# Optimization experiments

Hardware: AMD Instinct MI355X
Metric: run time of the kernel (lower is better)

Reference implementation:

```python
import jax, jax.numpy as jnp
import numpy as np

B, NN, HIS, MSG = 16, 1000, 12, 64
NODE_DIM, EDGE_DIM, META_DIM = 32, 16, 128
GAT_DIM = HIS * MSG            # 768
META_IN = NODE_DIM + GAT_DIM   # 800
N = B * NN                     # 16000 total nodes
E = 128000
NEG_SLOPE = 0.2


def setup_inputs() -> dict:
    key = jax.random.key(0)
    ks = jax.random.split(key, 16)
    def glorot(k, shape):
        fan_in = shape[0]
        lim = 1.0 / np.sqrt(fan_in)
        return jax.random.uniform(k, shape, jnp.float32, -lim, lim)
    return {
        "node_feature": jax.random.normal(ks[0], (B, NN, NODE_DIM), jnp.float32),
        "edge_attr": jax.random.normal(ks[1], (E, EDGE_DIM), jnp.float32),
        "message_feature": jax.random.normal(ks[2], (B, NN, HIS, MSG), jnp.float32),
        "edge_index": jax.random.randint(ks[3], (2, E), 0, N, jnp.int64) if jax.config.jax_enable_x64 else jax.random.randint(ks[3], (2, E), 0, N, jnp.int32),
        # node_learner / edge_learner
        "W_node": glorot(ks[4], (NODE_DIM, NODE_DIM)),
        "b_node": jnp.zeros((NODE_DIM,), jnp.float32),
        "W_edge": glorot(ks[5], (EDGE_DIM, EDGE_DIM)),
        "b_edge": jnp.zeros((EDGE_DIM,), jnp.float32),
        # GATConv(768, 768, heads=1, concat=False)
        "W_gat": glorot(ks[6], (GAT_DIM, GAT_DIM)),
        "att_src": glorot(ks[7], (GAT_DIM,)) * 0.1,
        "att_dst": glorot(ks[8], (GAT_DIM,)) * 0.1,
        "b_gat": jnp.zeros((GAT_DIM,), jnp.float32),
        # GNNConv([meta_in, meta_dim], dim=edge_dim)
        "W_nbr": glorot(ks[9], (2 * META_IN + EDGE_DIM, META_DIM)),
        "b_nbr": jnp.zeros((META_DIM,), jnp.float32),
        "W_self": glorot(ks[10], (META_IN, META_DIM)),
        "b_self": jnp.zeros((META_DIM,), jnp.float32),
    }


def reference(node_feature, edge_attr, message_feature, edge_index,
              W_node, b_node, W_edge, b_edge,
              W_gat, att_src, att_dst, b_gat,
              W_nbr, b_nbr, W_self, b_self):
    src, dst = edge_index[0], edge_index[1]  # j -> i

    # node / edge learners
    nf = (node_feature @ W_node + b_node).reshape(-1, NODE_DIM)        # [N, 32]
    ea = edge_attr @ W_edge + b_edge                                   # [E, 16]
    mf = message_feature.reshape(-1, GAT_DIM)                          # [N, 768]

    # --- GATConv (1 head, concat=False, add_self_loops=True, eval: no dropout) ---
    loops = jnp.arange(N, dtype=src.dtype)
    src_sl = jnp.concatenate([src, loops])
    dst_sl = jnp.concatenate([dst, loops])
    h = mf @ W_gat                                                     # [N, 768]
    a_src = h @ att_src                                                # [N]
    a_dst = h @ att_dst                                                # [N]
    alpha = jax.nn.leaky_relu(a_src[src_sl] + a_dst[dst_sl], NEG_SLOPE)  # [E+N]
    amax = jax.ops.segment_max(alpha, dst_sl, num_segments=N)
    ex = jnp.exp(alpha - amax[dst_sl])
    denom = jax.ops.segment_sum(ex, dst_sl, num_segments=N)
    coef = ex / denom[dst_sl]
    gat_out = jax.ops.segment_sum(h[src_sl] * coef[:, None], dst_sl, num_segments=N) + b_gat

    # --- meta input + GNNConv (aggr='add', batch_norm=False) ---
    x = jnp.concatenate([gat_out, nf], axis=-1)                        # [N, 800]
    z = jnp.concatenate([x[dst], x[src], ea], axis=-1)                 # [E, 1616]
    msg = z @ W_nbr + b_nbr                                            # [E, 128]
    agg = jax.ops.segment_sum(msg, dst, num_segments=N)                # [N, 128]
    out = agg + x @ W_self + b_self                                    # [N, 128]
    return out.reshape(-1, NN, META_DIM)                               # [B, 1000, 128]
```

## Files before the change

kernel.cpp:

```cpp
#include <hip/hip_runtime.h>

#define N_NODES 16000
#define N_EDGES 128000
#define GATD 768
#define NODED 32
#define EDGED 16
#define METAIN 800
#define METAD 128
#define YCOLS 384

typedef short s16x8 __attribute__((ext_vector_type(8)));
typedef float f32x4v __attribute__((ext_vector_type(4)));

__device__ __forceinline__ unsigned short f2bf(float f){
    unsigned u = __float_as_uint(f);
    return (unsigned short)((u + 0x7fffu + ((u >> 16) & 1u)) >> 16);
}
__device__ __forceinline__ float us2f(unsigned short u){ return __uint_as_float(((unsigned)u)<<16); }

__device__ __forceinline__ void gload16(const void* g, void* l){
    __builtin_amdgcn_global_load_lds((const __attribute__((address_space(1))) void*)g,
                                     (__attribute__((address_space(3))) void*)l, 16, 0, 0);
}

__global__ __launch_bounds__(256) void pack_all_kernel(const float* __restrict__ W_gat,
                                                       const float* __restrict__ W_nbr,
                                                       const float* __restrict__ W_self,
                                                       const float* __restrict__ W_edge,
                                                       const float* __restrict__ b_edge,
                                                       unsigned short* __restrict__ WgT,
                                                       unsigned short* __restrict__ WcatT,
                                                       float* __restrict__ W16g,
                                                       float* __restrict__ bbg){
    int bid = blockIdx.x, tid = threadIdx.x;
    if (bid < 144){
        __shared__ float t[64][65];
        int bi = bid / 12, bj = bid % 12;
        int r16 = tid >> 4, c4 = (tid & 15) * 4;
        #pragma unroll
        for (int it = 0; it < 4; ++it){
            int row = it*16 + r16;
            float4 v = *reinterpret_cast<const float4*>(W_gat + (size_t)(bi*64+row)*GATD + bj*64 + c4);
            t[row][c4+0]=v.x; t[row][c4+1]=v.y; t[row][c4+2]=v.z; t[row][c4+3]=v.w;
        }
        __syncthreads();
        #pragma unroll
        for (int it = 0; it < 4; ++it){
            int row = it*16 + r16;
            ushort4 o;
            o.x = f2bf(t[c4+0][row]); o.y = f2bf(t[c4+1][row]);
            o.z = f2bf(t[c4+2][row]); o.w = f2bf(t[c4+3][row]);
            *reinterpret_cast<ushort4*>(WgT + (size_t)(bj*64+row)*GATD + bi*64 + c4) = o;
        }
    } else if (bid < 1344){
        int idx = (bid-144)*256 + tid;
        int c = idx / METAIN, k = idx % METAIN;
        float v;
        if (c < 128)      v = W_nbr[(size_t)k*METAD + c];
        else if (c < 256) v = W_nbr[(size_t)(800+k)*METAD + (c-128)];
        else              v = W_self[(size_t)k*METAD + (c-256)];
        WcatT[idx] = f2bf(v);
    } else {
        int c = tid;
        if (c < 128){
            float w3[16];
            #pragma unroll
            for (int k = 0; k < 16; ++k) w3[k] = W_nbr[(size_t)(1600+k)*METAD + c];
            #pragma unroll
            for (int j = 0; j < 16; ++j){
                float s = 0.f;
                #pragma unroll
                for (int k = 0; k < 16; ++k) s += W_edge[j*16+k] * w3[k];
                W16g[j*128 + c] = s;
            }
            float bb = 0.f;
            #pragma unroll
            for (int k = 0; k < 16; ++k) bb += b_edge[k] * w3[k];
            bbg[c] = bb;
        }
    }
}

__global__ __launch_bounds__(256) void nf_kernel(const float* __restrict__ node_feature,
                                                 const float* __restrict__ W_node,
                                                 const float* __restrict__ b_node,
                                                 unsigned short* __restrict__ x_bf){
    __shared__ float Wn[1024];
    __shared__ float bn[32];
    int tid = threadIdx.x;
    for (int i = tid; i < 1024; i += 256) Wn[i] = W_node[i];
    if (tid < 32) bn[tid] = b_node[tid];
    __syncthreads();
    int idx = blockIdx.x*256 + tid;
    int n = idx >> 5, j = idx & 31;
    const float* row = node_feature + (size_t)n*NODED;
    float s = bn[j];
    #pragma unroll
    for (int k = 0; k < 32; ++k) s += row[k] * Wn[k*32 + j];
    x_bf[(size_t)n*METAIN + GATD + j] = f2bf(s);
}


__global__ __launch_bounds__(256) void deg_kernel(const int* __restrict__ dst, int* __restrict__ deg){
    int e = blockIdx.x*256 + threadIdx.x;
    atomicAdd(&deg[dst[e]], 1);
}

__global__ __launch_bounds__(1024) void scan_kernel(const int* __restrict__ deg,
                                                    int* __restrict__ rowstart,
                                                    int* __restrict__ cursor){
    __shared__ int part[1024];
    int t = threadIdx.x;
    int base = t * 16;
    int local[16];
    int s = 0;
    #pragma unroll
    for (int k = 0; k < 16; ++k){
        int idx = base + k;
        int v = (idx < N_NODES) ? deg[idx] : 0;
        local[k] = s; s += v;
    }
    part[t] = s;
    __syncthreads();
    for (int off = 1; off < 1024; off <<= 1){
        int v = 0;
        if (t >= off) v = part[t-off];
        __syncthreads();
        if (t >= off) part[t] += v;
        __syncthreads();
    }
    int excl = (t == 0) ? 0 : part[t-1];
    #pragma unroll
    for (int k = 0; k < 16; ++k){
        int idx = base + k;
        if (idx < N_NODES){ int rs = excl + local[k]; rowstart[idx] = rs; cursor[idx] = rs; }
    }
    if (t == 1023) rowstart[N_NODES] = part[1023];
}

__global__ __launch_bounds__(256) void csr_kernel(const int* __restrict__ dst,
                                                  int* __restrict__ cursor,
                                                  int* __restrict__ csr){
    int e = blockIdx.x*256 + threadIdx.x;
    int p = atomicAdd(&cursor[dst[e]], 1);
    csr[p] = e;
}


template<bool AF32, bool DOTS, bool BFOUT>
__global__ __launch_bounds__(256) void mfma_gemm_kernel(const float* __restrict__ A32,
                                                        const unsigned short* __restrict__ A16,
                                                        const unsigned short* __restrict__ Bt,
                                                        float* __restrict__ Cf,
                                                        unsigned short* __restrict__ Cb,
                                                        const float* __restrict__ att_src,
                                                        const float* __restrict__ att_dst,
                                                        float* __restrict__ a_srcO,
                                                        float* __restrict__ a_dstO,
                                                        int Ncols, int K){
    __shared__ __align__(16) unsigned short As[128*32];
    __shared__ __align__(16) unsigned short Bs[128*32];
    int tid = threadIdx.x;
    int wave = tid >> 6, lane = tid & 63;
    int rowBase = blockIdx.y * 128, colBase = blockIdx.x * 128;
    const float*          gA32p = AF32 ? A32 + (size_t)(rowBase + (tid>>2))*K + (tid&3)*8 : nullptr;
    const unsigned short* gA16p = AF32 ? nullptr : A16 + (size_t)(rowBase + (tid>>2))*K + (tid&3)*8;
    const unsigned short* gBp   = Bt + (size_t)(colBase + (tid>>2))*K + (tid&3)*8;
    char* lA = (char*)As + tid*16;
    char* lB = (char*)Bs + tid*16;
    int r0 = (wave>>1)*64, c0 = (wave&1)*64;
    int rl = lane & 15, koff = (lane>>4)*8;
    f32x4v acc[4][4] = {};
    for (int k0 = 0; k0 < K; k0 += 32){
        __syncthreads();
        gload16(gBp + k0,                  lB);
        gload16(gBp + (size_t)64*K + k0,   lB + 4096);
        if constexpr (AF32){
            float4 a0 = *reinterpret_cast<const float4*>(gA32p + k0);
            float4 a1 = *reinterpret_cast<const float4*>(gA32p + k0 + 4);
            float4 a2 = *reinterpret_cast<const float4*>(gA32p + (size_t)64*K + k0);
            float4 a3 = *reinterpret_cast<const float4*>(gA32p + (size_t)64*K + k0 + 4);
            union { unsigned short u[8]; s16x8 v; } p0, p1;
            p0.u[0]=f2bf(a0.x); p0.u[1]=f2bf(a0.y); p0.u[2]=f2bf(a0.z); p0.u[3]=f2bf(a0.w);
            p0.u[4]=f2bf(a1.x); p0.u[5]=f2bf(a1.y); p0.u[6]=f2bf(a1.z); p0.u[7]=f2bf(a1.w);
            p1.u[0]=f2bf(a2.x); p1.u[1]=f2bf(a2.y); p1.u[2]=f2bf(a2.z); p1.u[3]=f2bf(a2.w);
            p1.u[4]=f2bf(a3.x); p1.u[5]=f2bf(a3.y); p1.u[6]=f2bf(a3.z); p1.u[7]=f2bf(a3.w);
            *reinterpret_cast<s16x8*>(lA)        = p0.v;
            *reinterpret_cast<s16x8*>(lA + 4096) = p1.v;
        } else {
            gload16(gA16p + k0,                lA);
            gload16(gA16p + (size_t)64*K + k0, lA + 4096);
        }
        __syncthreads();
        s16x8 af[4], bfr[4];
        #pragma unroll
        for (int mi = 0; mi < 4; ++mi)
            af[mi] = *reinterpret_cast<const s16x8*>(&As[(r0 + mi*16 + rl)*32 + koff]);
        #pragma unroll
        for (int ni = 0; ni < 4; ++ni)
            bfr[ni] = *reinterpret_cast<const s16x8*>(&Bs[(c0 + ni*16 + rl)*32 + koff]);
        #pragma unroll
        for (int mi = 0; mi < 4; ++mi)
            #pragma unroll
            for (int ni = 0; ni < 4; ++ni)
                acc[mi][ni] = __builtin_amdgcn_mfma_f32_16x16x32_bf16(af[mi], bfr[ni], acc[mi][ni], 0, 0, 0);
    }
    int orow = rowBase + r0 + (lane>>4)*4;
    int ocol = colBase + c0 + rl;
    #pragma unroll
    for (int mi = 0; mi < 4; ++mi)
        #pragma unroll
        for (int ni = 0; ni < 4; ++ni){
            #pragma unroll
            for (int j = 0; j < 4; ++j){
                size_t idx = (size_t)(orow + mi*16 + j)*Ncols + ocol + ni*16;
                if constexpr (BFOUT) Cb[idx] = f2bf(acc[mi][ni][j]);
                else                 Cf[idx] = acc[mi][ni][j];
            }
        }
    if constexpr (DOTS){
        float as_c[4], ad_c[4];
        #pragma unroll
        for (int ni = 0; ni < 4; ++ni){
            int col = colBase + c0 + ni*16 + rl;
            as_c[ni] = att_src[col];
            ad_c[ni] = att_dst[col];
        }
        #pragma unroll
        for (int mi = 0; mi < 4; ++mi)
            #pragma unroll
            for (int j = 0; j < 4; ++j){
                float ps = 0.f, pd = 0.f;
                #pragma unroll
                for (int ni = 0; ni < 4; ++ni){
                    float v = acc[mi][ni][j];
                    ps += v * as_c[ni];
                    pd += v * ad_c[ni];
                }
                #pragma unroll
                for (int off = 8; off; off >>= 1){
                    ps += __shfl_xor(ps, off);
                    pd += __shfl_xor(pd, off);
                }
                if (rl == 0){
                    int r = rowBase + r0 + mi*16 + (lane>>4)*4 + j;
                    atomicAdd(&a_srcO[r], ps);
                    atomicAdd(&a_dstO[r], pd);
                }
            }
    }
}


__global__ __launch_bounds__(256) void gat_gather_kernel(const unsigned short* __restrict__ h_bf,
                                                         const float* __restrict__ a_src,
                                                         const float* __restrict__ a_dst,
                                                         const float* __restrict__ b_gat,
                                                         const int* __restrict__ src,
                                                         const int* __restrict__ rowstart,
                                                         const int* __restrict__ csr,
                                                         unsigned short* __restrict__ x_bf){
    int wv = threadIdx.x >> 6, lane = threadIdx.x & 63;
    int i = blockIdx.x*4 + wv;
    float adi = a_dst[i];
    float al = a_src[i] + adi;
    al = al > 0.f ? al : 0.2f*al;
    float ex_self = expf(al);
    const unsigned short* hi = h_bf + (size_t)i*GATD;
    float acc[12];
    #pragma unroll
    for (int c = 0; c < 3; ++c){
        ushort4 v = *reinterpret_cast<const ushort4*>(hi + c*256 + lane*4);
        acc[c*4+0] = ex_self*us2f(v.x); acc[c*4+1] = ex_self*us2f(v.y);
        acc[c*4+2] = ex_self*us2f(v.z); acc[c*4+3] = ex_self*us2f(v.w);
    }
    float dsum = ex_self;
    int rs = rowstart[i], re = rowstart[i+1];
    for (int p = rs; p < re; p += 64){
        int cnt = min(64, re - p);
        int sv = 0; float ev = 0.f;
        if (lane < cnt){
            int e = csr[p+lane];
            sv = src[e];
            float a = a_src[sv] + adi;
            a = a > 0.f ? a : 0.2f*a;
            ev = expf(a);
        }
        for (int j = 0; j < cnt; ++j){
            int   ss = __shfl(sv, j);
            float ww = __shfl(ev, j);
            dsum += ww;
            const unsigned short* hs = h_bf + (size_t)ss*GATD;
            #pragma unroll
            for (int c = 0; c < 3; ++c){
                ushort4 v = *reinterpret_cast<const ushort4*>(hs + c*256 + lane*4);
                acc[c*4+0] += ww*us2f(v.x); acc[c*4+1] += ww*us2f(v.y);
                acc[c*4+2] += ww*us2f(v.z); acc[c*4+3] += ww*us2f(v.w);
            }
        }
    }
    float inv = 1.f / dsum;
    unsigned short* xr = x_bf + (size_t)i*METAIN;
    #pragma unroll
    for (int c = 0; c < 3; ++c){
        float4 bg = *reinterpret_cast<const float4*>(b_gat + c*256 + lane*4);
        ushort4 o;
        o.x = f2bf(acc[c*4+0]*inv + bg.x); o.y = f2bf(acc[c*4+1]*inv + bg.y);
        o.z = f2bf(acc[c*4+2]*inv + bg.z); o.w = f2bf(acc[c*4+3]*inv + bg.w);
        *reinterpret_cast<ushort4*>(xr + c*256 + lane*4) = o;
    }
}


__global__ __launch_bounds__(128) void out_gather_kernel(const float* __restrict__ y,
                                                         const float* __restrict__ edge_attr,
                                                         const float* __restrict__ W16g,
                                                         const float* __restrict__ bbg,
                                                         const float* __restrict__ b_nbr,
                                                         const float* __restrict__ b_self,
                                                         const int* __restrict__ src,
                                                         const int* __restrict__ rowstart,
                                                         const int* __restrict__ csr,
                                                         float* __restrict__ out){
    __shared__ float W3[16*128];
    __shared__ int   s_src[32];
    __shared__ int   s_eid[32];
    __shared__ float s_ea[32*16];
    int i = blockIdx.x, c = threadIdx.x;
    #pragma unroll
    for (int k = 0; k < 16; ++k) W3[k*128 + c] = W16g[k*128 + c];
    int rs = rowstart[i], re = rowstart[i+1];
    int deg = re - rs;
    float acc = 0.f;
    for (int p = rs; p < re; p += 32){
        int cnt = min(32, re - p);
        __syncthreads();
        if (c < cnt){ int e = csr[p+c]; s_eid[c] = e; s_src[c] = src[e]; }
        __syncthreads();
        for (int idx = c; idx < cnt*16; idx += 128){
            int j = idx >> 4, k = idx & 15;
            s_ea[idx] = edge_attr[(size_t)s_eid[j]*EDGED + k];
        }
        __syncthreads();
        for (int j = 0; j < cnt; ++j){
            acc += y[(size_t)s_src[j]*YCOLS + 128 + c];
            float ez = 0.f;
            #pragma unroll
            for (int k = 0; k < 16; ++k) ez += s_ea[j*16 + k] * W3[k*128 + c];
            acc += ez;
        }
    }
    float y1 = y[(size_t)i*YCOLS + c];
    float ys = y[(size_t)i*YCOLS + 256 + c];
    float outv = (float)deg * (y1 + b_nbr[c] + bbg[c]) + acc + ys + b_self[c];
    out[(size_t)i*METAD + c] = outv;
}


extern "C" void kernel_launch(void* const* d_in, const int* in_sizes, int n_in,
                              void* d_out, int out_size, void* d_ws, size_t ws_size,
                              hipStream_t stream){
    const float* node_feature    = (const float*)d_in[0];
    const float* edge_attr       = (const float*)d_in[1];
    const float* message_feature = (const float*)d_in[2];
    const int*   edge_index      = (const int*)d_in[3];
    const float* W_node = (const float*)d_in[4];
    const float* b_node = (const float*)d_in[5];
    const float* W_edge = (const float*)d_in[6];
    const float* b_edge = (const float*)d_in[7];
    const float* W_gat  = (const float*)d_in[8];
    const float* att_src= (const float*)d_in[9];
    const float* att_dst= (const float*)d_in[10];
    const float* b_gat  = (const float*)d_in[11];
    const float* W_nbr  = (const float*)d_in[12];
    const float* b_nbr  = (const float*)d_in[13];
    const float* W_self = (const float*)d_in[14];
    const float* b_self = (const float*)d_in[15];
    float* out = (float*)d_out;

    char* wsb = (char*)d_ws;
    size_t off = 0;
    auto walloc = [&](size_t bytes)->void*{
        void* p = wsb + off;
        off = (off + bytes + 511) & ~(size_t)511;
        return p;
    };
    unsigned short* h_bf  = (unsigned short*)walloc((size_t)N_NODES*GATD*2);
    float* y              = (float*)walloc((size_t)N_NODES*YCOLS*4);
    unsigned short* x_bf  = (unsigned short*)walloc((size_t)N_NODES*METAIN*2);
    unsigned short* WgT   = (unsigned short*)walloc((size_t)GATD*GATD*2);
    unsigned short* WcatT = (unsigned short*)walloc((size_t)YCOLS*METAIN*2);
    float* W16g   = (float*)walloc(16*128*4);
    float* bbg    = (float*)walloc(128*4);
    float* zbase  = (float*)walloc((size_t)3*N_NODES*4);
    float* a_src  = zbase;
    float* a_dst  = zbase + N_NODES;
    int*   deg    = (int*)(zbase + 2*N_NODES);
    int* rowstart = (int*)walloc((size_t)(N_NODES+1)*4);
    int* cursor   = (int*)walloc((size_t)N_NODES*4);
    int* csr      = (int*)walloc((size_t)N_EDGES*4);

    const int* src = edge_index;
    const int* dst = edge_index + N_EDGES;

    hipMemsetAsync(zbase, 0, (size_t)3*N_NODES*4, stream);

    pack_all_kernel<<<1345, 256, 0, stream>>>(W_gat, W_nbr, W_self, W_edge, b_edge,
                                              WgT, WcatT, W16g, bbg);
    nf_kernel<<<(N_NODES*NODED)/256, 256, 0, stream>>>(node_feature, W_node, b_node, x_bf);
    deg_kernel<<<N_EDGES/256, 256, 0, stream>>>(dst, deg);
    scan_kernel<<<1, 1024, 0, stream>>>((const int*)deg, rowstart, cursor);
    csr_kernel<<<N_EDGES/256, 256, 0, stream>>>(dst, cursor, csr);

    mfma_gemm_kernel<true,true,true><<<dim3(GATD/128, N_NODES/128), 256, 0, stream>>>(
        message_feature, nullptr, WgT, nullptr, h_bf, att_src, att_dst, a_src, a_dst, GATD, GATD);

    gat_gather_kernel<<<N_NODES/4, 256, 0, stream>>>(h_bf, a_src, a_dst, b_gat, src, rowstart, csr, x_bf);

    mfma_gemm_kernel<false,false,false><<<dim3(YCOLS/128, N_NODES/128), 256, 0, stream>>>(
        nullptr, x_bf, WcatT, y, nullptr, nullptr, nullptr, nullptr, nullptr, YCOLS, METAIN);

    out_gather_kernel<<<N_NODES, 128, 0, stream>>>(y, edge_attr, W16g, bbg, b_nbr, b_self,
                                                   src, rowstart, csr, out);
}
```

Measured before the change: 311.3 us.

## Pre-convert message features to bf16 and use 512-thread GEMM blocks with row-major grid

Adds a separate kernel that converts message_feature from fp32 to bf16 once, so the GAT GEMM can stream both operands into LDS with direct global-to-LDS loads instead of converting in registers inside the K loop. The GEMM now uses 8 waves per 128x128 tile, each computing 64x32, which halves per-wave accumulators and raises occupancy. The grid is transposed so consecutive blocks walk rows while sharing the same B column tile. The cost is an extra pass that reads 49MB of fp32 and writes 25MB of bf16, plus a larger workspace.

```diff
diff --git a/kernel.cpp b/kernel.cpp
--- a/kernel.cpp
+++ b/kernel.cpp
@@ -21,6 +21,19 @@
 __device__ __forceinline__ void gload16(const void* g, void* l){
     __builtin_amdgcn_global_load_lds((const __attribute__((address_space(1))) void*)g,
                                      (__attribute__((address_space(3))) void*)l, 16, 0, 0);
+}
+
+
+__global__ __launch_bounds__(256) void conv_bf16_kernel(const float* __restrict__ in,
+                                                        unsigned short* __restrict__ out, int n8){
+    int i = blockIdx.x*256 + threadIdx.x;
+    if (i >= n8) return;
+    const float4* p = reinterpret_cast<const float4*>(in) + (size_t)i*2;
+    float4 a = p[0], b = p[1];
+    union { unsigned short u[8]; s16x8 v; } o;
+    o.u[0]=f2bf(a.x); o.u[1]=f2bf(a.y); o.u[2]=f2bf(a.z); o.u[3]=f2bf(a.w);
+    o.u[4]=f2bf(b.x); o.u[5]=f2bf(b.y); o.u[6]=f2bf(b.z); o.u[7]=f2bf(b.w);
+    reinterpret_cast<s16x8*>(out)[i] = o.v;
 }
 
 __global__ __launch_bounds__(256) void pack_all_kernel(const float* __restrict__ W_gat,
@@ -147,9 +160,8 @@
 }
 
 
-template<bool AF32, bool DOTS, bool BFOUT>
-__global__ __launch_bounds__(256) void mfma_gemm_kernel(const float* __restrict__ A32,
-                                                        const unsigned short* __restrict__ A16,
+template<bool DOTS, bool BFOUT>
+__global__ __launch_bounds__(512) void mfma_gemm_kernel(const unsigned short* __restrict__ A,
                                                         const unsigned short* __restrict__ Bt,
                                                         float* __restrict__ Cf,
                                                         unsigned short* __restrict__ Cb,
@@ -162,47 +174,30 @@
     __shared__ __align__(16) unsigned short Bs[128*32];
     int tid = threadIdx.x;
     int wave = tid >> 6, lane = tid & 63;
-    int rowBase = blockIdx.y * 128, colBase = blockIdx.x * 128;
-    const float*          gA32p = AF32 ? A32 + (size_t)(rowBase + (tid>>2))*K + (tid&3)*8 : nullptr;
-    const unsigned short* gA16p = AF32 ? nullptr : A16 + (size_t)(rowBase + (tid>>2))*K + (tid&3)*8;
-    const unsigned short* gBp   = Bt + (size_t)(colBase + (tid>>2))*K + (tid&3)*8;
+    int rowBase = blockIdx.x * 128, colBase = blockIdx.y * 128;
+    const unsigned short* gA = A  + (size_t)(rowBase + (tid>>2))*K + (tid&3)*8;
+    const unsigned short* gB = Bt + (size_t)(colBase + (tid>>2))*K + (tid&3)*8;
     char* lA = (char*)As + tid*16;
     char* lB = (char*)Bs + tid*16;
-    int r0 = (wave>>1)*64, c0 = (wave&1)*64;
+    int r0 = (wave>>2)*64, c0 = (wave&3)*32;
     int rl = lane & 15, koff = (lane>>4)*8;
-    f32x4v acc[4][4] = {};
+    f32x4v acc[4][2] = {};
     for (int k0 = 0; k0 < K; k0 += 32){
         __syncthreads();
-        gload16(gBp + k0,                  lB);
-        gload16(gBp + (size_t)64*K + k0,   lB + 4096);
-        if constexpr (AF32){
-            float4 a0 = *reinterpret_cast<const float4*>(gA32p + k0);
-            float4 a1 = *reinterpret_cast<const float4*>(gA32p + k0 + 4);
-            float4 a2 = *reinterpret_cast<const float4*>(gA32p + (size_t)64*K + k0);
-            float4 a3 = *reinterpret_cast<const float4*>(gA32p + (size_t)64*K + k0 + 4);
-            union { unsigned short u[8]; s16x8 v; } p0, p1;
-            p0.u[0]=f2bf(a0.x); p0.u[1]=f2bf(a0.y); p0.u[2]=f2bf(a0.z); p0.u[3]=f2bf(a0.w);
-            p0.u[4]=f2bf(a1.x); p0.u[5]=f2bf(a1.y); p0.u[6]=f2bf(a1.z); p0.u[7]=f2bf(a1.w);
-            p1.u[0]=f2bf(a2.x); p1.u[1]=f2bf(a2.y); p1.u[2]=f2bf(a2.z); p1.u[3]=f2bf(a2.w);
-            p1.u[4]=f2bf(a3.x); p1.u[5]=f2bf(a3.y); p1.u[6]=f2bf(a3.z); p1.u[7]=f2bf(a3.w);
-            *reinterpret_cast<s16x8*>(lA)        = p0.v;
-            *reinterpret_cast<s16x8*>(lA + 4096) = p1.v;
-        } else {
-            gload16(gA16p + k0,                lA);
-            gload16(gA16p + (size_t)64*K + k0, lA + 4096);
-        }
-        __syncthreads();
-        s16x8 af[4], bfr[4];
+        gload16(gA + k0, lA);
+        gload16(gB + k0, lB);
+        __syncthreads();
+        s16x8 af[4], bfr[2];
         #pragma unroll
         for (int mi = 0; mi < 4; ++mi)
             af[mi] = *reinterpret_cast<const s16x8*>(&As[(r0 + mi*16 + rl)*32 + koff]);
         #pragma unroll
-        for (int ni = 0; ni < 4; ++ni)
+        for (int ni = 0; ni < 2; ++ni)
             bfr[ni] = *reinterpret_cast<const s16x8*>(&Bs[(c0 + ni*16 + rl)*32 + koff]);
         #pragma unroll
         for (int mi = 0; mi < 4; ++mi)
             #pragma unroll
-            for (int ni = 0; ni < 4; ++ni)
+            for (int ni = 0; ni < 2; ++ni)
                 acc[mi][ni] = __builtin_amdgcn_mfma_f32_16x16x32_bf16(af[mi], bfr[ni], acc[mi][ni], 0, 0, 0);
     }
     int orow = rowBase + r0 + (lane>>4)*4;
@@ -210,7 +205,7 @@
     #pragma unroll
     for (int mi = 0; mi < 4; ++mi)
         #pragma unroll
-        for (int ni = 0; ni < 4; ++ni){
+        for (int ni = 0; ni < 2; ++ni){
             #pragma unroll
             for (int j = 0; j < 4; ++j){
                 size_t idx = (size_t)(orow + mi*16 + j)*Ncols + ocol + ni*16;
@@ -219,9 +214,9 @@
             }
         }
     if constexpr (DOTS){
-        float as_c[4], ad_c[4];
-        #pragma unroll
-        for (int ni = 0; ni < 4; ++ni){
+        float as_c[2], ad_c[2];
+        #pragma unroll
+        for (int ni = 0; ni < 2; ++ni){
             int col = colBase + c0 + ni*16 + rl;
             as_c[ni] = att_src[col];
             ad_c[ni] = att_dst[col];
@@ -232,7 +227,7 @@
             for (int j = 0; j < 4; ++j){
                 float ps = 0.f, pd = 0.f;
                 #pragma unroll
-                for (int ni = 0; ni < 4; ++ni){
+                for (int ni = 0; ni < 2; ++ni){
                     float v = acc[mi][ni][j];
                     ps += v * as_c[ni];
                     pd += v * ad_c[ni];
@@ -387,6 +382,7 @@
     };
     unsigned short* h_bf  = (unsigned short*)walloc((size_t)N_NODES*GATD*2);
     float* y              = (float*)walloc((size_t)N_NODES*YCOLS*4);
+    unsigned short* A_bf  = (unsigned short*)walloc((size_t)N_NODES*GATD*2);
     unsigned short* x_bf  = (unsigned short*)walloc((size_t)N_NODES*METAIN*2);
     unsigned short* WgT   = (unsigned short*)walloc((size_t)GATD*GATD*2);
     unsigned short* WcatT = (unsigned short*)walloc((size_t)YCOLS*METAIN*2);
@@ -405,6 +401,7 @@
 
     hipMemsetAsync(zbase, 0, (size_t)3*N_NODES*4, stream);
 
+    conv_bf16_kernel<<<(N_NODES*GATD/8 + 255)/256, 256, 0, stream>>>(message_feature, A_bf, N_NODES*GATD/8);
     pack_all_kernel<<<1345, 256, 0, stream>>>(W_gat, W_nbr, W_self, W_edge, b_edge,
                                               WgT, WcatT, W16g, bbg);
     nf_kernel<<<(N_NODES*NODED)/256, 256, 0, stream>>>(node_feature, W_node, b_node, x_bf);
@@ -412,13 +409,13 @@
     scan_kernel<<<1, 1024, 0, stream>>>((const int*)deg, rowstart, cursor);
     csr_kernel<<<N_EDGES/256, 256, 0, stream>>>(dst, cursor, csr);
 
-    mfma_gemm_kernel<true,true,true><<<dim3(GATD/128, N_NODES/128), 256, 0, stream>>>(
-        message_feature, nullptr, WgT, nullptr, h_bf, att_src, att_dst, a_src, a_dst, GATD, GATD);
+    mfma_gemm_kernel<true,true><<<dim3(N_NODES/128, GATD/128), 512, 0, stream>>>(
+        A_bf, WgT, nullptr, h_bf, att_src, att_dst, a_src, a_dst, GATD, GATD);
 
     gat_gather_kernel<<<N_NODES/4, 256, 0, stream>>>(h_bf, a_src, a_dst, b_gat, src, rowstart, csr, x_bf);
 
-    mfma_gemm_kernel<false,false,false><<<dim3(YCOLS/128, N_NODES/128), 256, 0, stream>>>(
-        nullptr, x_bf, WcatT, y, nullptr, nullptr, nullptr, nullptr, nullptr, YCOLS, METAIN);
+    mfma_gemm_kernel<false,false><<<dim3(N_NODES/128, YCOLS/128), 512, 0, stream>>>(
+        x_bf, WcatT, y, nullptr, nullptr, nullptr, nullptr, nullptr, YCOLS, METAIN);
 
     out_gather_kernel<<<N_NODES, 128, 0, stream>>>(y, edge_attr, W16g, bbg, b_nbr, b_self,
                                                    src, rowstart, csr, out);
```

New measurement: 305.6 us. Within noise of the previous version (-1.8%).
